# Kernel tuning notes

Hardware: AMD Instinct MI355X
Metric: run time of the kernel (lower is better)

Reference implementation:

```python
import jax, jax.numpy as jnp
import numpy as np

B = 4096        # batch
N_IN = 4096     # flattened input size
C = 128         # number of cores
A = 64          # axons (inputs) per core
O = 64          # neurons (outputs) per core
N_OUT = 1024    # number of output sources
CYCLES = 4      # ChipLatency
POOL_W = N_IN + 2 + C * O  # x cols | off(zero) | always_on(one) | core buffers


def setup_inputs() -> dict:
    key = jax.random.key(0)
    k1, k2, k3, k4 = jax.random.split(key, 4)
    x = jax.random.normal(k1, (B, N_IN), dtype=jnp.float32)
    # core_params[c] has shape (neurons_out, axons_in) = (O, A)
    W = jax.random.normal(k2, (C, O, A), dtype=jnp.float32) * 0.05
    # flat source index per (core, axon): encodes (is_input / is_off / is_always_on / buffer[core][neuron])
    axon_idx = jax.random.randint(k3, (C, A), 0, POOL_W, dtype=jnp.int32)
    out_idx = jax.random.randint(k4, (N_OUT,), 0, POOL_W, dtype=jnp.int32)
    return {"x": x, "W": W, "axon_idx": axon_idx, "out_idx": out_idx, "cycles": CYCLES}


def reference(x, W, axon_idx, out_idx, cycles):
    b = x.shape[0]
    c, o, a = W.shape
    zero_col = jnp.zeros((b, 1), x.dtype)   # is_off sources
    one_col = jnp.ones((b, 1), x.dtype)     # is_always_on sources
    buffers = jnp.zeros((b, c * o), x.dtype)  # all core buffers, flattened core-major

    def make_pool(buf):
        return jnp.concatenate([x, zero_col, one_col, buf], axis=1)  # (b, POOL_W)

    for _ in range(cycles):
        pool = make_pool(buffers)
        inp = pool[:, axon_idx]  # (b, c, a) fused get_signal_tensor gather
        # buffer[c] = relu(input_signals[c] @ core_matrix[c]) == relu(W[c] @ inp[c].T).T
        buffers = jax.nn.relu(jnp.einsum('coa,bca->bco', W, inp)).reshape(b, c * o)

    pool = make_pool(buffers)
    return pool[:, out_idx]  # (b, N_OUT) output_sources gather
```

## Files before the change

### kernel.cpp

```cpp
#include <hip/hip_runtime.h>

typedef __attribute__((ext_vector_type(8))) short short8;
typedef __attribute__((ext_vector_type(8))) __bf16 bf16x8;
typedef __attribute__((ext_vector_type(4))) float f32x4;
typedef __attribute__((ext_vector_type(4))) unsigned short ushort4_t;
typedef __attribute__((ext_vector_type(4))) unsigned int uint4_t;

#define NB   4096
#define NIN  4096
#define NX   4098
#define NC   128
#define NO   64
#define NA   64
#define NOUT 1024

__device__ __forceinline__ unsigned short f2bf(float f) {
  unsigned b = __builtin_bit_cast(unsigned, f);
  b += 0x7FFFu + ((b >> 16) & 1u);
  return (unsigned short)(b >> 16);
}
__device__ __forceinline__ float bf2f(unsigned short u) {
  return __builtin_bit_cast(float, (unsigned)u << 16);
}

__global__ __launch_bounds__(256) void prep_kernel(
    const float* __restrict__ x, const float* __restrict__ W,
    unsigned short* __restrict__ xT, unsigned short* __restrict__ Wb) {
  int bid = blockIdx.x, t = threadIdx.x;
  if (bid < 4096) {
    __shared__ unsigned short tile[64][68];
    int b0 = (bid >> 6) << 6, n0 = (bid & 63) << 6;
    int r = t >> 4, c4 = (t & 15) << 2;
#pragma unroll
    for (int rr = 0; rr < 4; ++rr) {
      int row = r + rr * 16;
      float4 v = *(const float4*)(x + (size_t)(b0 + row) * NIN + n0 + c4);
      tile[row][c4 + 0] = f2bf(v.x);
      tile[row][c4 + 1] = f2bf(v.y);
      tile[row][c4 + 2] = f2bf(v.z);
      tile[row][c4 + 3] = f2bf(v.w);
    }
    __syncthreads();
#pragma unroll
    for (int rr = 0; rr < 4; ++rr) {
      int nl = r + rr * 16;
      ushort4_t o;
      o.x = tile[c4 + 0][nl];
      o.y = tile[c4 + 1][nl];
      o.z = tile[c4 + 2][nl];
      o.w = tile[c4 + 3][nl];
      *(ushort4_t*)(xT + (size_t)(n0 + nl) * NB + b0 + c4) = o;
    }
  } else if (bid < 4096 + 256) {
    size_t i0 = (size_t)(bid - 4096) * 2048 + (size_t)t * 8;
    float4 v0 = *(const float4*)(W + i0);
    float4 v1 = *(const float4*)(W + i0 + 4);
    ushort4_t a, b;
    a.x = f2bf(v0.x); a.y = f2bf(v0.y); a.z = f2bf(v0.z); a.w = f2bf(v0.w);
    b.x = f2bf(v1.x); b.y = f2bf(v1.y); b.z = f2bf(v1.z); b.w = f2bf(v1.w);
    *(ushort4_t*)(Wb + i0) = a;
    *(ushort4_t*)(Wb + i0 + 4) = b;
  } else {
    int e = (bid - 4352) * 1024 + t * 4;
    int row = e >> 12, col = e & 4095;
    unsigned short val = (row == 0) ? (unsigned short)0 : (unsigned short)0x3F80;
    ushort4_t o = {val, val, val, val};
    *(ushort4_t*)(xT + (size_t)(NIN + row) * NB + col) = o;
  }
}

__global__ __launch_bounds__(1024) void mask_kernel(
    const int* __restrict__ axon, const int* __restrict__ oidx,
    unsigned char* __restrict__ gmask, unsigned char* __restrict__ omask) {
  int t = threadIdx.x;
  for (int i = t; i < NC * NO; i += 1024) { gmask[i] = 0; omask[i] = 0; }
  __syncthreads();
  for (int i = t; i < NC * NA; i += 1024) {
    int idx = axon[i];
    if (idx >= NX) gmask[idx - NX] = 1;
  }
  if (t < NOUT) {
    int idx = oidx[t];
    if (idx >= NX) omask[idx - NX] = 1;
  }
}

template <int MODE>
__global__ __launch_bounds__(512) void cycle_kernel(
    const unsigned short* __restrict__ xT, const unsigned short* __restrict__ Wb,
    const unsigned short* __restrict__ bufPrev, unsigned short* __restrict__ bufNext,
    const int* __restrict__ axon, const unsigned char* __restrict__ mask,
    int first) {
  __shared__ __align__(16) unsigned short SM[64 * 520];
  int c = blockIdx.y;
  int t = threadIdx.x;
  int b0 = blockIdx.x << 9;
  const int* arow = axon + (c << 6);

  int lane = t & 63, w = t >> 6;
  int ln = lane & 15, g = lane >> 4;

  {
    int ao = w, bo = lane;
    const int* ar = arow + ao * 8;
    uint4_t rows[8];
#pragma unroll
    for (int r = 0; r < 8; ++r) {
      int idx = ar[r];
      const unsigned short* s = nullptr;
      if (idx < NX)      s = xT + (size_t)idx * NB;
      else if (!first)   s = bufPrev + (size_t)(idx - NX) * NB;
      if (s) rows[r] = *(const uint4_t*)(s + b0 + bo * 8);
      else   rows[r] = (uint4_t)(0u);
    }
    unsigned lo[4][4], hi[4][4];
#pragma unroll
    for (int p = 0; p < 4; ++p)
#pragma unroll
      for (int k = 0; k < 4; ++k) {
        unsigned wi = rows[2 * p][k], wj = rows[2 * p + 1][k];
        lo[p][k] = __builtin_amdgcn_perm(wj, wi, 0x05040100u);
        hi[p][k] = __builtin_amdgcn_perm(wj, wi, 0x07060302u);
      }
#pragma unroll
    for (int e = 0; e < 8; ++e) {
      int k = e >> 1;
      uint4_t col;
      if (e & 1) { col[0] = hi[0][k]; col[1] = hi[1][k]; col[2] = hi[2][k]; col[3] = hi[3][k]; }
      else       { col[0] = lo[0][k]; col[1] = lo[1][k]; col[2] = lo[2][k]; col[3] = lo[3][k]; }
      int b = bo * 8 + e;
      int sw = ao ^ (b & 7) ^ ((b >> 5) & 7);
      *(uint4_t*)&SM[b * 64 + (sw << 3)] = col;
    }
  }
  __syncthreads();

  const unsigned short* wrow = Wb + ((size_t)c << 12);

  bool grp[4];
#pragma unroll
  for (int j = 0; j < 4; ++j) {
    if (MODE == 1) grp[j] = __any((int)(mask[(c << 6) + j * 16 + ln] != 0));
    else           grp[j] = true;
  }

  f32x4 acc[4][4];
#pragma unroll
  for (int i = 0; i < 4; ++i)
#pragma unroll
    for (int j = 0; j < 4; ++j) acc[i][j] = (f32x4)(0.f);

#pragma unroll
  for (int ks = 0; ks < 2; ++ks) {
    short8 ag[4];
#pragma unroll
    for (int i = 0; i < 4; ++i) {
      int bl = (w << 6) + (i << 4) + ln;
      int c8 = (ks << 2) + g;
      int sw = c8 ^ (bl & 7) ^ ((bl >> 5) & 7);
      ag[i] = *(const short8*)&SM[bl * 64 + (sw << 3)];
    }
#pragma unroll
    for (int j = 0; j < 4; ++j) {
      if (!grp[j]) continue;
      short8 bw = *(const short8*)(wrow + ((size_t)(j * 16 + ln) << 6) + ks * 32 + g * 8);
#pragma unroll
      for (int i = 0; i < 4; ++i)
        acc[i][j] = __builtin_amdgcn_mfma_f32_16x16x32_bf16(
            __builtin_bit_cast(bf16x8, ag[i]), __builtin_bit_cast(bf16x8, bw),
            acc[i][j], 0, 0, 0);
    }
  }

  __syncthreads();
#pragma unroll
  for (int j = 0; j < 4; ++j) {
    int o = j * 16 + ln;
#pragma unroll
    for (int i = 0; i < 4; ++i) {
      ushort4_t pk;
#pragma unroll
      for (int r = 0; r < 4; ++r) pk[r] = f2bf(fmaxf(acc[i][j][r], 0.f));
      *(ushort4_t*)&SM[o * 520 + (w << 6) + (i << 4) + (g << 2)] = pk;
    }
  }
  __syncthreads();
#pragma unroll
  for (int it = 0; it < 8; ++it) {
    int row = it * 8 + w;
    if (mask[(c << 6) + row] == 0) continue;
    uint4_t v = *(const uint4_t*)&SM[row * 520 + (lane << 3)];
    *(uint4_t*)(bufNext + ((size_t)((c << 6) + row)) * NB + b0 + (lane << 3)) = v;
  }
}

__global__ __launch_bounds__(256) void final_kernel(
    const unsigned short* __restrict__ xT, const unsigned short* __restrict__ bufFin,
    const int* __restrict__ out_idx, float* __restrict__ out) {
  __shared__ unsigned short tile[256][66];
  int j0 = blockIdx.x << 6, b0 = blockIdx.y << 8;
  int t = threadIdx.x;
  {
    int jl = t >> 2, bq = t & 3;
    int idx = out_idx[j0 + jl];
    const unsigned short* src = (idx < NX) ? xT + (size_t)idx * NB
                                           : bufFin + (size_t)(idx - NX) * NB;
    int jcol = jl ^ (bq << 4);
#pragma unroll
    for (int k = 0; k < 8; ++k) {
      short8 v = *(const short8*)(src + b0 + bq * 64 + k * 8);
#pragma unroll
      for (int m = 0; m < 8; ++m)
        tile[bq * 64 + k * 8 + m][jcol] = (unsigned short)v[m];
    }
  }
  __syncthreads();
  {
    int j = t & 63, ws = t >> 6;
#pragma unroll
    for (int bb = 0; bb < 64; ++bb) {
      int b = bb * 4 + ws;
      int jc = j ^ ((b >> 6) << 4);
      out[(size_t)(b0 + b) * NOUT + j0 + j] = bf2f(tile[b][jc]);
    }
  }
}

extern "C" void kernel_launch(void* const* d_in, const int* in_sizes, int n_in,
                              void* d_out, int out_size, void* d_ws, size_t ws_size,
                              hipStream_t stream) {
  const float* x    = (const float*)d_in[0];
  const float* W    = (const float*)d_in[1];
  const int*   axon = (const int*)d_in[2];
  const int*   oidx = (const int*)d_in[3];
  float* out = (float*)d_out;

  const size_t XT_BYTES  = (size_t)NX * NB * 2;
  const size_t WB_BYTES  = (size_t)NC * NO * NA * 2;
  const size_t BUF_BYTES = (size_t)NC * NO * NB * 2;
  const size_t MASK_B    = 8192;
  if (ws_size < XT_BYTES + WB_BYTES + 2 * BUF_BYTES + 2 * MASK_B) return;

  char* ws = (char*)d_ws;
  unsigned short* xT    = (unsigned short*)ws;
  unsigned short* Wb    = (unsigned short*)(ws + XT_BYTES);
  unsigned short* bufA  = (unsigned short*)(ws + XT_BYTES + WB_BYTES);
  unsigned short* bufB  = (unsigned short*)(ws + XT_BYTES + WB_BYTES + BUF_BYTES);
  unsigned char*  gmask = (unsigned char*)(ws + XT_BYTES + WB_BYTES + 2 * BUF_BYTES);
  unsigned char*  omask = gmask + MASK_B;

  prep_kernel<<<4360, 256, 0, stream>>>(x, W, xT, Wb);
  mask_kernel<<<1, 1024, 0, stream>>>(axon, oidx, gmask, omask);
  dim3 cg(NB / 512, NC);
  cycle_kernel<0><<<cg, 512, 0, stream>>>(xT, Wb, bufB, bufA, axon, gmask, 1);
  cycle_kernel<0><<<cg, 512, 0, stream>>>(xT, Wb, bufA, bufB, axon, gmask, 0);
  cycle_kernel<0><<<cg, 512, 0, stream>>>(xT, Wb, bufB, bufA, axon, gmask, 0);
  cycle_kernel<1><<<cg, 512, 0, stream>>>(xT, Wb, bufA, bufB, axon, omask, 0);
  final_kernel<<<dim3(NOUT / 64, NB / 256), 256, 0, stream>>>(xT, bufB, oidx, out);
}
```

Baseline: 139.7 us.

## Split cycle kernel batch tile into two half-chunks with prefetch overlap

The cycle kernel now handles its 512-batch slice as two 256-column chunks using two LDS regions. Global loads for the second chunk are issued before the first chunk's MFMA compute and epilogue, so memory latency can overlap with compute. Each lane now loads 4 rows instead of 8, which lowers register pressure, and launch bounds request 4 blocks per SM. The LDS epilogue layout switches to an XOR swizzle, and the final stores shrink to 8-byte writes, so global store coalescing gets narrower.

```diff
diff --git a/kernel.cpp b/kernel.cpp
--- a/kernel.cpp
+++ b/kernel.cpp
@@ -5,6 +5,7 @@
 typedef __attribute__((ext_vector_type(4))) float f32x4;
 typedef __attribute__((ext_vector_type(4))) unsigned short ushort4_t;
 typedef __attribute__((ext_vector_type(4))) unsigned int uint4_t;
+typedef __attribute__((ext_vector_type(2))) unsigned int uint2_t;
 
 #define NB   4096
 #define NIN  4096
@@ -13,6 +14,7 @@
 #define NO   64
 #define NA   64
 #define NOUT 1024
+#define NROW (NC * NO)
 
 __device__ __forceinline__ unsigned short f2bf(float f) {
   unsigned b = __builtin_bit_cast(unsigned, f);
@@ -73,7 +75,7 @@
     const int* __restrict__ axon, const int* __restrict__ oidx,
     unsigned char* __restrict__ gmask, unsigned char* __restrict__ omask) {
   int t = threadIdx.x;
-  for (int i = t; i < NC * NO; i += 1024) { gmask[i] = 0; omask[i] = 0; }
+  for (int i = t; i < NROW; i += 1024) { gmask[i] = 0; omask[i] = 0; }
   __syncthreads();
   for (int i = t; i < NC * NA; i += 1024) {
     int idx = axon[i];
@@ -86,112 +88,134 @@
 }
 
 template <int MODE>
-__global__ __launch_bounds__(512) void cycle_kernel(
+__global__ __launch_bounds__(512, 4) void cycle_kernel(
     const unsigned short* __restrict__ xT, const unsigned short* __restrict__ Wb,
     const unsigned short* __restrict__ bufPrev, unsigned short* __restrict__ bufNext,
     const int* __restrict__ axon, const unsigned char* __restrict__ mask,
     int first) {
-  __shared__ __align__(16) unsigned short SM[64 * 520];
+  __shared__ __align__(16) unsigned short R0[128 * 128];
+  __shared__ __align__(16) unsigned short R1[128 * 128];
   int c = blockIdx.y;
   int t = threadIdx.x;
   int b0 = blockIdx.x << 9;
-  const int* arow = axon + (c << 6);
-
   int lane = t & 63, w = t >> 6;
   int ln = lane & 15, g = lane >> 4;
-
-  {
-    int ao = w, bo = lane;
-    const int* ar = arow + ao * 8;
-    uint4_t rows[8];
-#pragma unroll
-    for (int r = 0; r < 8; ++r) {
-      int idx = ar[r];
-      const unsigned short* s = nullptr;
-      if (idx < NX)      s = xT + (size_t)idx * NB;
-      else if (!first)   s = bufPrev + (size_t)(idx - NX) * NB;
-      if (s) rows[r] = *(const uint4_t*)(s + b0 + bo * 8);
-      else   rows[r] = (uint4_t)(0u);
-    }
-    unsigned lo[4][4], hi[4][4];
-#pragma unroll
-    for (int p = 0; p < 4; ++p)
-#pragma unroll
-      for (int k = 0; k < 4; ++k) {
-        unsigned wi = rows[2 * p][k], wj = rows[2 * p + 1][k];
-        lo[p][k] = __builtin_amdgcn_perm(wj, wi, 0x05040100u);
-        hi[p][k] = __builtin_amdgcn_perm(wj, wi, 0x07060302u);
-      }
-#pragma unroll
-    for (int e = 0; e < 8; ++e) {
-      int k = e >> 1;
-      uint4_t col;
-      if (e & 1) { col[0] = hi[0][k]; col[1] = hi[1][k]; col[2] = hi[2][k]; col[3] = hi[3][k]; }
-      else       { col[0] = lo[0][k]; col[1] = lo[1][k]; col[2] = lo[2][k]; col[3] = lo[3][k]; }
-      int b = bo * 8 + e;
-      int sw = ao ^ (b & 7) ^ ((b >> 5) & 7);
-      *(uint4_t*)&SM[b * 64 + (sw << 3)] = col;
-    }
-  }
-  __syncthreads();
+  int g5 = t >> 5, lane5 = t & 31;
+  int ao = g5 >> 1, h = g5 & 1;
+  const int* arow = axon + (c << 6);
+
+  const unsigned short* src[4];
+#pragma unroll
+  for (int r = 0; r < 4; ++r) {
+    int idx = arow[g5 * 4 + r];
+    const unsigned short* s = nullptr;
+    if (idx < NX)      s = xT + (size_t)idx * NB;
+    else if (!first)   s = bufPrev + (size_t)(idx - NX) * NB;
+    src[r] = s;
+  }
 
   const unsigned short* wrow = Wb + ((size_t)c << 12);
-
   bool grp[4];
 #pragma unroll
-  for (int j = 0; j < 4; ++j) {
-    if (MODE == 1) grp[j] = __any((int)(mask[(c << 6) + j * 16 + ln] != 0));
-    else           grp[j] = true;
-  }
-
-  f32x4 acc[4][4];
-#pragma unroll
-  for (int i = 0; i < 4; ++i)
-#pragma unroll
-    for (int j = 0; j < 4; ++j) acc[i][j] = (f32x4)(0.f);
-
-#pragma unroll
-  for (int ks = 0; ks < 2; ++ks) {
-    short8 ag[4];
-#pragma unroll
-    for (int i = 0; i < 4; ++i) {
-      int bl = (w << 6) + (i << 4) + ln;
-      int c8 = (ks << 2) + g;
-      int sw = c8 ^ (bl & 7) ^ ((bl >> 5) & 7);
-      ag[i] = *(const short8*)&SM[bl * 64 + (sw << 3)];
-    }
+  for (int j = 0; j < 4; ++j)
+    grp[j] = (MODE == 1) ? __any((int)(mask[(c << 6) + j * 16 + ln] != 0)) : true;
+
+  auto transpose_write = [&](unsigned short* Rk, uint4_t* L) {
+#pragma unroll
+    for (int k = 0; k < 4; ++k) {
+      unsigned lo01 = __builtin_amdgcn_perm(L[1][k], L[0][k], 0x05040100u);
+      unsigned hi01 = __builtin_amdgcn_perm(L[1][k], L[0][k], 0x07060302u);
+      unsigned lo23 = __builtin_amdgcn_perm(L[3][k], L[2][k], 0x05040100u);
+      unsigned hi23 = __builtin_amdgcn_perm(L[3][k], L[2][k], 0x07060302u);
+#pragma unroll
+      for (int hb = 0; hb < 2; ++hb) {
+        int bl = lane5 * 8 + 2 * k + hb;
+        int sw = ao ^ (bl & 7) ^ ((bl >> 5) & 7);
+        uint2_t col;
+        col[0] = hb ? hi01 : lo01;
+        col[1] = hb ? hi23 : lo23;
+        *(uint2_t*)&Rk[bl * 64 + (sw << 3) + (h << 2)] = col;
+      }
+    }
+  };
+
+  auto compute = [&](const unsigned short* Rk, f32x4 (&acc)[2][4]) {
+#pragma unroll
+    for (int i = 0; i < 2; ++i)
+#pragma unroll
+      for (int j = 0; j < 4; ++j) acc[i][j] = (f32x4)(0.f);
+#pragma unroll
+    for (int ks = 0; ks < 2; ++ks) {
+      short8 ag[2];
+#pragma unroll
+      for (int i = 0; i < 2; ++i) {
+        int bl = (w << 5) + (i << 4) + ln;
+        int c8 = (ks << 2) + g;
+        int sw = c8 ^ (bl & 7) ^ ((bl >> 5) & 7);
+        ag[i] = *(const short8*)&Rk[bl * 64 + (sw << 3)];
+      }
+#pragma unroll
+      for (int j = 0; j < 4; ++j) {
+        if (MODE == 1 && !grp[j]) continue;
+        short8 bw = *(const short8*)(wrow + ((size_t)(j * 16 + ln) << 6) + ks * 32 + g * 8);
+#pragma unroll
+        for (int i = 0; i < 2; ++i)
+          acc[i][j] = __builtin_amdgcn_mfma_f32_16x16x32_bf16(
+              __builtin_bit_cast(bf16x8, ag[i]), __builtin_bit_cast(bf16x8, bw),
+              acc[i][j], 0, 0, 0);
+      }
+    }
+  };
+
+  auto epilogue = [&](unsigned short* Rk, f32x4 (&acc)[2][4], int ck) {
+    char* OS = (char*)Rk;
 #pragma unroll
     for (int j = 0; j < 4; ++j) {
-      if (!grp[j]) continue;
-      short8 bw = *(const short8*)(wrow + ((size_t)(j * 16 + ln) << 6) + ks * 32 + g * 8);
-#pragma unroll
-      for (int i = 0; i < 4; ++i)
-        acc[i][j] = __builtin_amdgcn_mfma_f32_16x16x32_bf16(
-            __builtin_bit_cast(bf16x8, ag[i]), __builtin_bit_cast(bf16x8, bw),
-            acc[i][j], 0, 0, 0);
-    }
-  }
-
-  __syncthreads();
-#pragma unroll
-  for (int j = 0; j < 4; ++j) {
-    int o = j * 16 + ln;
-#pragma unroll
-    for (int i = 0; i < 4; ++i) {
-      ushort4_t pk;
-#pragma unroll
-      for (int r = 0; r < 4; ++r) pk[r] = f2bf(fmaxf(acc[i][j][r], 0.f));
-      *(ushort4_t*)&SM[o * 520 + (w << 6) + (i << 4) + (g << 2)] = pk;
-    }
-  }
-  __syncthreads();
-#pragma unroll
-  for (int it = 0; it < 8; ++it) {
-    int row = it * 8 + w;
-    if (mask[(c << 6) + row] == 0) continue;
-    uint4_t v = *(const uint4_t*)&SM[row * 520 + (lane << 3)];
-    *(uint4_t*)(bufNext + ((size_t)((c << 6) + row)) * NB + b0 + (lane << 3)) = v;
-  }
+      int o = j * 16 + ln;
+      int sz = (o & 7) << 4;
+#pragma unroll
+      for (int i = 0; i < 2; ++i) {
+        ushort4_t pk;
+#pragma unroll
+        for (int r = 0; r < 4; ++r) pk[r] = f2bf(fmaxf(acc[i][j][r], 0.f));
+        int inner = (w << 6) + (i << 5) + (g << 3);
+        *(ushort4_t*)(OS + o * 512 + (inner ^ sz)) = pk;
+      }
+    }
+    __syncthreads();
+#pragma unroll
+    for (int it = 0; it < 8; ++it) {
+      int row = it * 8 + w;
+      if (mask[(c << 6) + row] == 0) continue;
+      ushort4_t v = *(const ushort4_t*)(OS + row * 512 + ((lane * 8) ^ ((row & 7) << 4)));
+      *(ushort4_t*)(bufNext + ((size_t)((c << 6) + row)) * NB + b0 + ck * 256 + (lane << 2)) = v;
+    }
+  };
+
+  const uint4_t Z = (uint4_t)0u;
+  f32x4 acc[2][4];
+
+  uint4_t L0[4];
+#pragma unroll
+  for (int r = 0; r < 4; ++r)
+    L0[r] = src[r] ? *(const uint4_t*)(src[r] + b0 + lane5 * 8) : Z;
+  transpose_write(R0, L0);
+  __syncthreads();
+
+  uint4_t L1[4];
+#pragma unroll
+  for (int r = 0; r < 4; ++r)
+    L1[r] = src[r] ? *(const uint4_t*)(src[r] + b0 + 256 + lane5 * 8) : Z;
+
+  compute(R0, acc);
+  __syncthreads();
+  epilogue(R0, acc, 0);
+
+  transpose_write(R1, L1);
+  __syncthreads();
+  compute(R1, acc);
+  __syncthreads();
+  epilogue(R1, acc, 1);
 }
 
 __global__ __launch_bounds__(256) void final_kernel(
@@ -237,17 +261,17 @@
 
   const size_t XT_BYTES  = (size_t)NX * NB * 2;
   const size_t WB_BYTES  = (size_t)NC * NO * NA * 2;
-  const size_t BUF_BYTES = (size_t)NC * NO * NB * 2;
+  const size_t BUF_BYTES = (size_t)NROW * NB * 2;
   const size_t MASK_B    = 8192;
   if (ws_size < XT_BYTES + WB_BYTES + 2 * BUF_BYTES + 2 * MASK_B) return;
 
-  char* ws = (char*)d_ws;
-  unsigned short* xT    = (unsigned short*)ws;
-  unsigned short* Wb    = (unsigned short*)(ws + XT_BYTES);
-  unsigned short* bufA  = (unsigned short*)(ws + XT_BYTES + WB_BYTES);
-  unsigned short* bufB  = (unsigned short*)(ws + XT_BYTES + WB_BYTES + BUF_BYTES);
-  unsigned char*  gmask = (unsigned char*)(ws + XT_BYTES + WB_BYTES + 2 * BUF_BYTES);
-  unsigned char*  omask = gmask + MASK_B;
+  char* p = (char*)d_ws;
+  unsigned short* xT    = (unsigned short*)p;  p += XT_BYTES;
+  unsigned short* Wb    = (unsigned short*)p;  p += WB_BYTES;
+  unsigned short* bufA  = (unsigned short*)p;  p += BUF_BYTES;
+  unsigned short* bufB  = (unsigned short*)p;  p += BUF_BYTES;
+  unsigned char*  gmask = (unsigned char*)p;   p += MASK_B;
+  unsigned char*  omask = (unsigned char*)p;
 
   prep_kernel<<<4360, 256, 0, stream>>>(x, W, xT, Wb);
   mask_kernel<<<1, 1024, 0, stream>>>(axon, oidx, gmask, omask);
```

After: 166.3 us. +19.0%, slower.
